# Optimization experiments

Hardware: AMD Instinct MI355X
Metric: run time of the kernel (lower is better)

## Reference

```python
import jax, jax.numpy as jnp
import numpy as np
import math

B, S, D = 2, 2048, 1024
N_HEAD = 16
EPS = 1e-6

def setup_inputs() -> dict:
    key = jax.random.key(0)
    ks = jax.random.split(key, 12)
    def lin(k):
        kw, kb = jax.random.split(k)
        scale = 1.0 / math.sqrt(D)
        W = jax.random.uniform(kw, (D, D), jnp.float32, -scale, scale)
        b = jax.random.uniform(kb, (D,), jnp.float32, -scale, scale)
        return W, b
    Wq, bq = lin(ks[0]); Wk, bk = lin(ks[1]); Wv, bv = lin(ks[2]); Wo, bo = lin(ks[3])
    return {
        'query': jax.random.normal(ks[4], (B, S, D), jnp.float32),
        'key':   jax.random.normal(ks[5], (B, S, D), jnp.float32),
        'value': jax.random.normal(ks[6], (B, S, D), jnp.float32),
        'mask':  jnp.ones((B, S, S), jnp.int32),
        'Wq': Wq, 'bq': bq, 'Wk': Wk, 'bk': bk, 'Wv': Wv, 'bv': bv,
        'Wo': Wo, 'bo': bo,
        'gamma': jnp.ones((D,), jnp.float32),
        'beta':  jnp.zeros((D,), jnp.float32),
    }

def reference(query, key, value, mask, Wq, bq, Wk, bk, Wv, bv, Wo, bo, gamma, beta):
    b, s, dm = query.shape
    h = N_HEAD
    d = dm // h
    residual = query
    # projections (torch Linear: x @ W.T + b) -> [b, h, s, d]
    def proj(x, W, bias):
        return (x @ W.T + bias).reshape(b, -1, h, d).transpose(0, 2, 1, 3)
    q = proj(query, Wq, bq)
    k = proj(key, Wk, bk)
    v = proj(value, Wv, bv)
    scores = jnp.einsum('bhqd,bhkd->bhqk', q, k) / jnp.sqrt(jnp.float32(d))
    scores = jnp.where(mask[:, None, :, :] == 0, jnp.float32(-1e9), scores)
    p_attn = jax.nn.softmax(scores, axis=-1)  # dropout is identity in eval/reference
    x = jnp.einsum('bhqk,bhkd->bhqd', p_attn, v)
    x = x.transpose(0, 2, 1, 3).reshape(b, -1, h * d)
    x = x @ Wo.T + bo
    x = x + residual
    # LayerNorm with unbiased std and (std + eps) denominator, as in source
    mean = jnp.mean(x, axis=-1, keepdims=True)
    std = jnp.std(x, axis=-1, keepdims=True, ddof=1)
    return gamma * (x - mean) / (std + EPS) + beta
```

## Files before the change

kernel.cpp:

```cpp
#include <hip/hip_runtime.h>
#include <hip/hip_bf16.h>
#include <math.h>
#include <stdint.h>

#define BATCH 2
#define SEQ   2048
#define DMODEL 1024
#define NHEAD 16
#define HDIM  64
#define NROWS (BATCH*SEQ)
#define EPS   1e-6f
#define QSCALE 0.1803368801111204f

typedef float f32x4 __attribute__((ext_vector_type(4)));
typedef short s16x8 __attribute__((ext_vector_type(8)));

#define OFF_XQ 0
#define OFF_XK 4194304
#define OFF_XV 8388608
#define OFF_WQ 12582912
#define OFF_WK 13631488
#define OFF_WV 14680064
#define OFF_WO 15728640
#define OFF_QB 16777216
#define OFF_KB 20971520
#define OFF_VT 25165824
#define OFF_CM 29360128
#define OFF_MS 29884416

__device__ __forceinline__ unsigned short f2bf(float x) {
    unsigned int u = __builtin_bit_cast(unsigned int, x);
    u += 0x7fff + ((u >> 16) & 1);
    return (unsigned short)(u >> 16);
}

__device__ __forceinline__ void gl_lds16(const void* g, void* l) {
    __builtin_amdgcn_global_load_lds(
        (const __attribute__((address_space(1))) unsigned int*)g,
        (__attribute__((address_space(3))) unsigned int*)(unsigned int)(unsigned long long)l,
        16, 0, 0);
}

__global__ __launch_bounds__(256) void conv_all_kernel(
    const float* __restrict__ q, const float* __restrict__ k, const float* __restrict__ v,
    const float* __restrict__ wq, const float* __restrict__ wk, const float* __restrict__ wv,
    const float* __restrict__ wo, unsigned short* __restrict__ ws)
{
    if (blockIdx.x == 0 && threadIdx.x < 32)
        ((unsigned int*)(ws + OFF_MS))[threadIdx.x] = 0;
    size_t t = ((size_t)blockIdx.x * 256 + threadIdx.x) * 4;
    const float* src; unsigned short* dst; size_t off;
    if (t < 4194304)       { src = q;  dst = ws + OFF_XQ; off = t; }
    else if (t < 8388608)  { src = k;  dst = ws + OFF_XK; off = t - 4194304; }
    else if (t < 12582912) { src = v;  dst = ws + OFF_XV; off = t - 8388608; }
    else if (t < 13631488) { src = wq; dst = ws + OFF_WQ; off = t - 12582912; }
    else if (t < 14680064) { src = wk; dst = ws + OFF_WK; off = t - 13631488; }
    else if (t < 15728640) { src = wv; dst = ws + OFF_WV; off = t - 14680064; }
    else                   { src = wo; dst = ws + OFF_WO; off = t - 15728640; }
    float4 x = *(const float4*)&src[off];
    ushort4 o;
    o.x = f2bf(x.x); o.y = f2bf(x.y); o.z = f2bf(x.z); o.w = f2bf(x.w);
    *(ushort4*)&dst[off] = o;
}

__global__ __launch_bounds__(256) void mask_compress_kernel(
    const int* __restrict__ mask, unsigned long long* __restrict__ cm,
    unsigned int* __restrict__ msum)
{
    int t = blockIdx.x * 256 + threadIdx.x;
    int s  = t & 2047;
    int kb = (t >> 11) & 31;
    int b  = t >> 16;
    const int* mp = mask + ((size_t)b * SEQ + s) * SEQ + kb * 64;
    unsigned long long bits = 0;
    #pragma unroll
    for (int i = 0; i < 16; i++) {
        int4 m4 = *(const int4*)&mp[i * 4];
        unsigned long long nib =
            (unsigned long long)((m4.x != 0) | ((m4.y != 0) << 1) |
                                 ((m4.z != 0) << 2) | ((m4.w != 0) << 3));
        bits |= nib << (i * 4);
    }
    cm[((size_t)b * 32 + kb) * SEQ + s] = bits;
    if (bits != ~0ull)
        atomicOr(&msum[(b << 4) | (s >> 7)], 1u << kb);
}

__device__ __forceinline__ void gemm_body(
    const unsigned short* A, const unsigned short* W, int r0, int c0,
    unsigned short* As, unsigned short* Bs, f32x4 acc[4][4])
{
    const int tid  = threadIdx.x;
    const int wave = tid >> 6, lane = tid & 63;
    const int quad = lane >> 4, l15 = lane & 15;
    const int wr = wave >> 1, wc = wave & 1;
    for (int k0 = 0; k0 < DMODEL; k0 += 64) {
        __syncthreads();
        #pragma unroll
        for (int r = 0; r < 4; r++) {
            int f = r * 4096 + tid * 16;
            int row = f >> 7, cb = f & 127;
            gl_lds16((const char*)A + (size_t)(r0 + row) * 2048 + k0 * 2 + cb,
                     (char*)As + r * 4096 + wave * 1024);
            gl_lds16((const char*)W + (size_t)(c0 + row) * 2048 + k0 * 2 + cb,
                     (char*)Bs + r * 4096 + wave * 1024);
        }
        __syncthreads();
        #pragma unroll
        for (int ks = 0; ks < 2; ks++) {
            s16x8 a[4], b[4];
            #pragma unroll
            for (int mt = 0; mt < 4; mt++)
                a[mt] = *(const s16x8*)((const char*)As + (wr*64 + mt*16 + l15) * 128 + ks*64 + quad*16);
            #pragma unroll
            for (int nt = 0; nt < 4; nt++)
                b[nt] = *(const s16x8*)((const char*)Bs + (wc*64 + nt*16 + l15) * 128 + ks*64 + quad*16);
            #pragma unroll
            for (int mt = 0; mt < 4; mt++)
                #pragma unroll
                for (int nt = 0; nt < 4; nt++)
                    acc[mt][nt] = __builtin_amdgcn_mfma_f32_16x16x32_bf16(a[mt], b[nt], acc[mt][nt], 0, 0, 0);
        }
    }
}

__global__ __launch_bounds__(256) void qkv_gemm_kernel(
    unsigned short* __restrict__ ws,
    const float* __restrict__ bq, const float* __restrict__ bk, const float* __restrict__ bv)
{
    __shared__ __align__(16) unsigned short As[8192];
    __shared__ __align__(16) unsigned short Bs[8192];
    const int z = blockIdx.z;
    const unsigned short *A, *W;
    int r0, c0;
    if (z != 2) {
        A = ws + (size_t)z * 4194304;
        W = ws + OFF_WQ + (size_t)z * 1048576;
        r0 = blockIdx.x * 128; c0 = blockIdx.y * 128;
    } else {
        A = ws + OFF_WV;
        W = ws + OFF_XV;
        r0 = blockIdx.y * 128; c0 = blockIdx.x * 128;
    }
    const float* bias = (z == 0) ? bq : (z == 1 ? bk : bv);
    unsigned short* outp = ws + OFF_QB + (size_t)z * 4194304;
    const float scale = (z == 0) ? QSCALE : 1.0f;

    f32x4 acc[4][4] = {};
    gemm_body(A, W, r0, c0, As, Bs, acc);

    const int lane = threadIdx.x & 63, wave = threadIdx.x >> 6;
    const int quad = lane >> 4, l15 = lane & 15;
    const int wr = wave >> 1, wc = wave & 1;
    if (z != 2) {
        float bias_v[4];
        #pragma unroll
        for (int nt = 0; nt < 4; nt++) bias_v[nt] = bias[c0 + wc*64 + nt*16 + l15];
        #pragma unroll
        for (int mt = 0; mt < 4; mt++) {
            #pragma unroll
            for (int nt = 0; nt < 4; nt++) {
                int c = c0 + wc*64 + nt*16 + l15;
                int hh = c >> 6, dd = c & 63;
                #pragma unroll
                for (int reg = 0; reg < 4; reg++) {
                    int r = r0 + wr*64 + mt*16 + quad*4 + reg;
                    int bb = r >> 11, ss = r & (SEQ - 1);
                    float val = (acc[mt][nt][reg] + bias_v[nt]) * scale;
                    outp[(((size_t)(bb*NHEAD + hh)) * SEQ + ss) * HDIM + dd] = f2bf(val);
                }
            }
        }
    } else {
        #pragma unroll
        for (int mt = 0; mt < 4; mt++) {
            #pragma unroll
            for (int reg = 0; reg < 4; reg++) {
                int f = r0 + wr*64 + mt*16 + quad*4 + reg;
                int hh = f >> 6, dd = f & 63;
                float bfv = bias[f];
                #pragma unroll
                for (int nt = 0; nt < 4; nt++) {
                    int r = c0 + wc*64 + nt*16 + l15;
                    int bb = r >> 11, ss = r & (SEQ - 1);
                    outp[(((size_t)(bb*NHEAD + hh)) * HDIM + dd) * SEQ + ss] =
                        f2bf(acc[mt][nt][reg] + bfv);
                }
            }
        }
    }
}

__global__ __launch_bounds__(256) void oproj_gemm_kernel(
    const unsigned short* __restrict__ ws, const float* __restrict__ bo,
    const float* __restrict__ resid, float* __restrict__ outf)
{
    __shared__ __align__(16) unsigned short As[8192];
    __shared__ __align__(16) unsigned short Bs[8192];
    const unsigned short* A = ws + OFF_XQ;
    const unsigned short* W = ws + OFF_WO;
    const int r0 = blockIdx.x * 128, c0 = blockIdx.y * 128;

    f32x4 acc[4][4] = {};
    gemm_body(A, W, r0, c0, (unsigned short*)As, (unsigned short*)Bs, acc);

    const int lane = threadIdx.x & 63, wave = threadIdx.x >> 6;
    const int quad = lane >> 4, l15 = lane & 15;
    const int wr = wave >> 1, wc = wave & 1;
    #pragma unroll
    for (int mt = 0; mt < 4; mt++) {
        #pragma unroll
        for (int nt = 0; nt < 4; nt++) {
            int c = c0 + wc*64 + nt*16 + l15;
            float bv = bo[c];
            #pragma unroll
            for (int reg = 0; reg < 4; reg++) {
                int r = r0 + wr*64 + mt*16 + quad*4 + reg;
                size_t idx = (size_t)r * DMODEL + c;
                outf[idx] = acc[mt][nt][reg] + bv + resid[idx];
            }
        }
    }
}

__global__ __launch_bounds__(512) void attn_mfma_kernel(
    const unsigned short* __restrict__ ws,
    const unsigned long long* __restrict__ cmask,
    const unsigned int* __restrict__ msum,
    unsigned short* __restrict__ ab)
{
    const int tid  = threadIdx.x;
    const int wave = tid >> 6, lane = tid & 63;
    const int quad = lane >> 4, l15 = lane & 15;
    const int h = blockIdx.y, b = blockIdx.z;
    const int qw = blockIdx.x * 128 + wave * 16;

    const char* qh = (const char*)(ws + OFF_QB + ((size_t)(b*NHEAD + h)) * SEQ * HDIM);
    const char* kh = (const char*)(ws + OFF_KB + ((size_t)(b*NHEAD + h)) * SEQ * HDIM);
    const char* vh = (const char*)(ws + OFF_VT + ((size_t)(b*NHEAD + h)) * SEQ * HDIM);

    __shared__ __align__(16) char Ks[2][8192];
    __shared__ __align__(16) char Vs[2][8192];
    __shared__ __align__(16) unsigned short Pl[8][16 * 72];
    unsigned short* Pw = Pl[wave];

    const unsigned int chunkflags = msum[(b << 4) | blockIdx.x];

    const int srow = tid >> 3;
    const int sgrp = ((tid & 7) - srow) & 7;

    #define STAGE(bf, k0)                                                       \
        do {                                                                    \
            gl_lds16(kh + (size_t)((k0) + srow) * 128 + sgrp * 16,              \
                     Ks[bf] + wave * 1024);                                     \
            gl_lds16(vh + (size_t)srow * 4096 + (size_t)(k0) * 2 + sgrp * 16,   \
                     Vs[bf] + wave * 1024);                                     \
        } while (0)

    s16x8 qa[2];
    #pragma unroll
    for (int ks = 0; ks < 2; ks++)
        qa[ks] = *(const s16x8*)(qh + (size_t)(qw + l15) * 128 + ks*64 + quad*16);

    s16x8 onesf;
    {
        short so = (short)0x3F80;
        if (l15 == 0) onesf = (s16x8){so, so, so, so, so, so, so, so};
        else          onesf = (s16x8){0, 0, 0, 0, 0, 0, 0, 0};
    }

    f32x4 o[4], lsum = {0.f, 0.f, 0.f, 0.f};
    #pragma unroll
    for (int nt = 0; nt < 4; nt++) o[nt] = (f32x4){0.f, 0.f, 0.f, 0.f};

    STAGE(0, 0);
    int bf = 0;
    for (int k0 = 0; k0 < SEQ; k0 += 64) {
        __syncthreads();
        if (k0 + 64 < SEQ) STAGE(bf ^ 1, k0 + 64);

        const char* Kb = Ks[bf];
        const char* Vb = Vs[bf];
        f32x4 s[4];
        #pragma unroll
        for (int nt = 0; nt < 4; nt++) {
            int key = nt*16 + l15;
            s16x8 kf0 = *(const s16x8*)(Kb + key*128 + ((quad     + key) & 7) * 16);
            s16x8 kf1 = *(const s16x8*)(Kb + key*128 + ((4 + quad + key) & 7) * 16);
            f32x4 z = {0.f, 0.f, 0.f, 0.f};
            s[nt] = __builtin_amdgcn_mfma_f32_16x16x32_bf16(qa[0], kf0, z, 0, 0, 0);
            s[nt] = __builtin_amdgcn_mfma_f32_16x16x32_bf16(qa[1], kf1, s[nt], 0, 0, 0);
        }
        if (chunkflags & (1u << (k0 >> 6))) {
            const unsigned long long* cmp =
                cmask + ((size_t)b*32 + (k0 >> 6)) * SEQ + qw + quad*4;
            #pragma unroll
            for (int reg = 0; reg < 4; reg++) {
                unsigned long long cm = cmp[reg];
                if (cm != ~0ull) {
                    #pragma unroll
                    for (int nt = 0; nt < 4; nt++) {
                        int n = nt*16 + l15;
                        if (!((cm >> n) & 1)) s[nt][reg] = -1e9f;
                    }
                }
            }
        }
        #pragma unroll
        for (int nt = 0; nt < 4; nt++)
            #pragma unroll
            for (int reg = 0; reg < 4; reg++) {
                float pv = exp2f(s[nt][reg]);
                Pw[(quad*4 + reg) * 72 + nt*16 + l15] =
                    (unsigned short)(__builtin_bit_cast(unsigned int, pv) >> 16);
            }
        #pragma unroll
        for (int ks = 0; ks < 2; ks++) {
            s16x8 pa = *(const s16x8*)((const char*)Pw + l15 * 144 + ks*64 + quad*16);
            lsum = __builtin_amdgcn_mfma_f32_16x16x32_bf16(pa, onesf, lsum, 0, 0, 0);
            #pragma unroll
            for (int nt = 0; nt < 4; nt++) {
                int d = nt*16 + l15;
                s16x8 vf = *(const s16x8*)(Vb + d*128 + ((ks*4 + quad + d) & 7) * 16);
                o[nt] = __builtin_amdgcn_mfma_f32_16x16x32_bf16(pa, vf, o[nt], 0, 0, 0);
            }
        }
        bf ^= 1;
    }
    #undef STAGE
    #pragma unroll
    for (int reg = 0; reg < 4; reg++) {
        float lv = __shfl(lsum[reg], lane & 48);
        float inv = 1.f / lv;
        int sg = qw + quad*4 + reg;
        #pragma unroll
        for (int nt = 0; nt < 4; nt++) {
            size_t idx = ((size_t)b * SEQ + sg) * DMODEL + h*HDIM + nt*16 + l15;
            ab[idx] = f2bf(o[nt][reg] * inv);
        }
    }
}

__global__ __launch_bounds__(256) void ln_kernel(
    float* __restrict__ x, const float* __restrict__ gamma,
    const float* __restrict__ beta)
{
    const int row = blockIdx.x;
    const int tid = threadIdx.x;
    float4 vals = *(const float4*)&x[(size_t)row * DMODEL + tid * 4];
    float s  = vals.x + vals.y + vals.z + vals.w;
    float ss = vals.x*vals.x + vals.y*vals.y + vals.z*vals.z + vals.w*vals.w;
    #pragma unroll
    for (int off = 32; off > 0; off >>= 1) {
        s  += __shfl_down(s, off);
        ss += __shfl_down(ss, off);
    }
    __shared__ float sbuf[4], ssbuf[4];
    __shared__ float mean_s, inv_s;
    if ((tid & 63) == 0) { sbuf[tid >> 6] = s; ssbuf[tid >> 6] = ss; }
    __syncthreads();
    if (tid == 0) {
        float S1 = 0.f, S2 = 0.f;
        #pragma unroll
        for (int i = 0; i < 4; i++) { S1 += sbuf[i]; S2 += ssbuf[i]; }
        float mean = S1 * (1.0f / DMODEL);
        float var  = (S2 - (float)DMODEL * mean * mean) * (1.0f / (DMODEL - 1));
        float sd   = sqrtf(fmaxf(var, 0.f));
        mean_s = mean;
        inv_s  = 1.f / (sd + EPS);
    }
    __syncthreads();
    float4 g  = *(const float4*)&gamma[tid * 4];
    float4 bt = *(const float4*)&beta[tid * 4];
    float4 o;
    o.x = g.x * (vals.x - mean_s) * inv_s + bt.x;
    o.y = g.y * (vals.y - mean_s) * inv_s + bt.y;
    o.z = g.z * (vals.z - mean_s) * inv_s + bt.z;
    o.w = g.w * (vals.w - mean_s) * inv_s + bt.w;
    *(float4*)&x[(size_t)row * DMODEL + tid * 4] = o;
}

extern "C" void kernel_launch(void* const* d_in, const int* in_sizes, int n_in,
                              void* d_out, int out_size, void* d_ws, size_t ws_size,
                              hipStream_t stream) {
    const float* query = (const float*)d_in[0];
    const float* key   = (const float*)d_in[1];
    const float* value = (const float*)d_in[2];
    const int*   mask  = (const int*)d_in[3];
    const float* Wq = (const float*)d_in[4];  const float* bq = (const float*)d_in[5];
    const float* Wk = (const float*)d_in[6];  const float* bk = (const float*)d_in[7];
    const float* Wv = (const float*)d_in[8];  const float* bv = (const float*)d_in[9];
    const float* Wo = (const float*)d_in[10]; const float* bo = (const float*)d_in[11];
    const float* gamma = (const float*)d_in[12];
    const float* beta  = (const float*)d_in[13];
    float* out = (float*)d_out;

    unsigned short* ws = (unsigned short*)d_ws;
    unsigned long long* cmask = (unsigned long long*)(ws + OFF_CM);
    unsigned int* msum = (unsigned int*)(ws + OFF_MS);

    conv_all_kernel<<<16384, 256, 0, stream>>>(query, key, value, Wq, Wk, Wv, Wo, ws);
    mask_compress_kernel<<<512, 256, 0, stream>>>(mask, cmask, msum);
    qkv_gemm_kernel<<<dim3(32, 8, 3), 256, 0, stream>>>(ws, bq, bk, bv);
    attn_mfma_kernel<<<dim3(SEQ/128, NHEAD, BATCH), 512, 0, stream>>>(ws, cmask, msum, ws + OFF_XQ);
    oproj_gemm_kernel<<<dim3(32, 8), 256, 0, stream>>>(ws, bo, query, out);
    ln_kernel<<<NROWS, 256, 0, stream>>>(out, gamma, beta);
}
```

Baseline: 289.4 us.

## Fuse mask compression into conversion, split-K out-proj, widen attention wave tiles

Result: slower. 314.0 us (+8.5%).

```diff
diff --git a/kernel.cpp b/kernel.cpp
--- a/kernel.cpp
+++ b/kernel.cpp
@@ -44,10 +44,30 @@
 __global__ __launch_bounds__(256) void conv_all_kernel(
     const float* __restrict__ q, const float* __restrict__ k, const float* __restrict__ v,
     const float* __restrict__ wq, const float* __restrict__ wk, const float* __restrict__ wv,
-    const float* __restrict__ wo, unsigned short* __restrict__ ws)
-{
-    if (blockIdx.x == 0 && threadIdx.x < 32)
-        ((unsigned int*)(ws + OFF_MS))[threadIdx.x] = 0;
+    const float* __restrict__ wo, unsigned short* __restrict__ ws,
+    const int* __restrict__ mask, unsigned long long* __restrict__ cm,
+    unsigned int* __restrict__ msum)
+{
+    if (blockIdx.x >= 16384) {
+        int t = (blockIdx.x - 16384) * 256 + threadIdx.x;
+        int s  = t & 2047;
+        int kb = (t >> 11) & 31;
+        int b  = t >> 16;
+        const int* mp = mask + ((size_t)b * SEQ + s) * SEQ + kb * 64;
+        unsigned long long bits = 0;
+        #pragma unroll
+        for (int i = 0; i < 16; i++) {
+            int4 m4 = *(const int4*)&mp[i * 4];
+            unsigned long long nib =
+                (unsigned long long)((m4.x != 0) | ((m4.y != 0) << 1) |
+                                     ((m4.z != 0) << 2) | ((m4.w != 0) << 3));
+            bits |= nib << (i * 4);
+        }
+        cm[((size_t)b * 32 + kb) * SEQ + s] = bits;
+        if (bits != ~0ull)
+            atomicOr(&msum[(b << 4) | (s >> 7)], 1u << kb);
+        return;
+    }
     size_t t = ((size_t)blockIdx.x * 256 + threadIdx.x) * 4;
     const float* src; unsigned short* dst; size_t off;
     if (t < 4194304)       { src = q;  dst = ws + OFF_XQ; off = t; }
@@ -63,38 +83,15 @@
     *(ushort4*)&dst[off] = o;
 }
 
-__global__ __launch_bounds__(256) void mask_compress_kernel(
-    const int* __restrict__ mask, unsigned long long* __restrict__ cm,
-    unsigned int* __restrict__ msum)
-{
-    int t = blockIdx.x * 256 + threadIdx.x;
-    int s  = t & 2047;
-    int kb = (t >> 11) & 31;
-    int b  = t >> 16;
-    const int* mp = mask + ((size_t)b * SEQ + s) * SEQ + kb * 64;
-    unsigned long long bits = 0;
-    #pragma unroll
-    for (int i = 0; i < 16; i++) {
-        int4 m4 = *(const int4*)&mp[i * 4];
-        unsigned long long nib =
-            (unsigned long long)((m4.x != 0) | ((m4.y != 0) << 1) |
-                                 ((m4.z != 0) << 2) | ((m4.w != 0) << 3));
-        bits |= nib << (i * 4);
-    }
-    cm[((size_t)b * 32 + kb) * SEQ + s] = bits;
-    if (bits != ~0ull)
-        atomicOr(&msum[(b << 4) | (s >> 7)], 1u << kb);
-}
-
 __device__ __forceinline__ void gemm_body(
     const unsigned short* A, const unsigned short* W, int r0, int c0,
-    unsigned short* As, unsigned short* Bs, f32x4 acc[4][4])
+    int kbeg, int kend, unsigned short* As, unsigned short* Bs, f32x4 acc[4][4])
 {
     const int tid  = threadIdx.x;
     const int wave = tid >> 6, lane = tid & 63;
     const int quad = lane >> 4, l15 = lane & 15;
     const int wr = wave >> 1, wc = wave & 1;
-    for (int k0 = 0; k0 < DMODEL; k0 += 64) {
+    for (int k0 = kbeg; k0 < kend; k0 += 64) {
         __syncthreads();
         #pragma unroll
         for (int r = 0; r < 4; r++) {
@@ -147,7 +144,7 @@
     const float scale = (z == 0) ? QSCALE : 1.0f;
 
     f32x4 acc[4][4] = {};
-    gemm_body(A, W, r0, c0, As, Bs, acc);
+    gemm_body(A, W, r0, c0, 0, DMODEL, As, Bs, acc);
 
     const int lane = threadIdx.x & 63, wave = threadIdx.x >> 6;
     const int quad = lane >> 4, l15 = lane & 15;
@@ -192,18 +189,20 @@
 }
 
 __global__ __launch_bounds__(256) void oproj_gemm_kernel(
-    const unsigned short* __restrict__ ws, const float* __restrict__ bo,
-    const float* __restrict__ resid, float* __restrict__ outf)
+    const unsigned short* __restrict__ ws,
+    float* __restrict__ p0, float* __restrict__ p1)
 {
     __shared__ __align__(16) unsigned short As[8192];
     __shared__ __align__(16) unsigned short Bs[8192];
     const unsigned short* A = ws + OFF_XQ;
     const unsigned short* W = ws + OFF_WO;
     const int r0 = blockIdx.x * 128, c0 = blockIdx.y * 128;
+    const int z = blockIdx.z;
 
     f32x4 acc[4][4] = {};
-    gemm_body(A, W, r0, c0, (unsigned short*)As, (unsigned short*)Bs, acc);
-
+    gemm_body(A, W, r0, c0, z * 512, z * 512 + 512, As, Bs, acc);
+
+    float* outp = z ? p1 : p0;
     const int lane = threadIdx.x & 63, wave = threadIdx.x >> 6;
     const int quad = lane >> 4, l15 = lane & 15;
     const int wr = wave >> 1, wc = wave & 1;
@@ -212,18 +211,16 @@
         #pragma unroll
         for (int nt = 0; nt < 4; nt++) {
             int c = c0 + wc*64 + nt*16 + l15;
-            float bv = bo[c];
             #pragma unroll
             for (int reg = 0; reg < 4; reg++) {
                 int r = r0 + wr*64 + mt*16 + quad*4 + reg;
-                size_t idx = (size_t)r * DMODEL + c;
-                outf[idx] = acc[mt][nt][reg] + bv + resid[idx];
-            }
-        }
-    }
-}
-
-__global__ __launch_bounds__(512) void attn_mfma_kernel(
+                outp[(size_t)r * DMODEL + c] = acc[mt][nt][reg];
+            }
+        }
+    }
+}
+
+__global__ __launch_bounds__(256) void attn_mfma_kernel(
     const unsigned short* __restrict__ ws,
     const unsigned long long* __restrict__ cmask,
     const unsigned int* __restrict__ msum,
@@ -233,7 +230,7 @@
     const int wave = tid >> 6, lane = tid & 63;
     const int quad = lane >> 4, l15 = lane & 15;
     const int h = blockIdx.y, b = blockIdx.z;
-    const int qw = blockIdx.x * 128 + wave * 16;
+    const int qw = blockIdx.x * 128 + wave * 32;
 
     const char* qh = (const char*)(ws + OFF_QB + ((size_t)(b*NHEAD + h)) * SEQ * HDIM);
     const char* kh = (const char*)(ws + OFF_KB + ((size_t)(b*NHEAD + h)) * SEQ * HDIM);
@@ -241,26 +238,32 @@
 
     __shared__ __align__(16) char Ks[2][8192];
     __shared__ __align__(16) char Vs[2][8192];
-    __shared__ __align__(16) unsigned short Pl[8][16 * 72];
+    __shared__ __align__(16) unsigned short Pl[4][32 * 72];
     unsigned short* Pw = Pl[wave];
 
     const unsigned int chunkflags = msum[(b << 4) | blockIdx.x];
 
     const int srow = tid >> 3;
-    const int sgrp = ((tid & 7) - srow) & 7;
-
-    #define STAGE(bf, k0)                                                       \
-        do {                                                                    \
-            gl_lds16(kh + (size_t)((k0) + srow) * 128 + sgrp * 16,              \
-                     Ks[bf] + wave * 1024);                                     \
-            gl_lds16(vh + (size_t)srow * 4096 + (size_t)(k0) * 2 + sgrp * 16,   \
-                     Vs[bf] + wave * 1024);                                     \
+    const int g0   = ((tid & 7) - srow) & 7;
+
+    #define STAGE(bf, k0)                                                          \
+        do {                                                                       \
+            gl_lds16(kh + (size_t)((k0) + srow) * 128 + g0 * 16,                   \
+                     Ks[bf] + wave * 1024);                                        \
+            gl_lds16(kh + (size_t)((k0) + srow + 32) * 128 + g0 * 16,              \
+                     Ks[bf] + 4096 + wave * 1024);                                 \
+            gl_lds16(vh + (size_t)srow * 4096 + (size_t)(k0) * 2 + g0 * 16,        \
+                     Vs[bf] + wave * 1024);                                        \
+            gl_lds16(vh + (size_t)(srow + 32) * 4096 + (size_t)(k0) * 2 + g0 * 16, \
+                     Vs[bf] + 4096 + wave * 1024);                                 \
         } while (0)
 
-    s16x8 qa[2];
+    s16x8 qa[2][2];
     #pragma unroll
-    for (int ks = 0; ks < 2; ks++)
-        qa[ks] = *(const s16x8*)(qh + (size_t)(qw + l15) * 128 + ks*64 + quad*16);
+    for (int mt = 0; mt < 2; mt++)
+        #pragma unroll
+        for (int ks = 0; ks < 2; ks++)
+            qa[mt][ks] = *(const s16x8*)(qh + (size_t)(qw + mt*16 + l15) * 128 + ks*64 + quad*16);
 
     s16x8 onesf;
     {
@@ -269,9 +272,13 @@
         else          onesf = (s16x8){0, 0, 0, 0, 0, 0, 0, 0};
     }
 
-    f32x4 o[4], lsum = {0.f, 0.f, 0.f, 0.f};
+    f32x4 o[2][4], lsum[2];
     #pragma unroll
-    for (int nt = 0; nt < 4; nt++) o[nt] = (f32x4){0.f, 0.f, 0.f, 0.f};
+    for (int mt = 0; mt < 2; mt++) {
+        lsum[mt] = (f32x4){0.f, 0.f, 0.f, 0.f};
+        #pragma unroll
+        for (int nt = 0; nt < 4; nt++) o[mt][nt] = (f32x4){0.f, 0.f, 0.f, 0.f};
+    }
 
     STAGE(0, 0);
     int bf = 0;
@@ -281,73 +288,99 @@
 
         const char* Kb = Ks[bf];
         const char* Vb = Vs[bf];
-        f32x4 s[4];
+        f32x4 s[2][4];
         #pragma unroll
         for (int nt = 0; nt < 4; nt++) {
             int key = nt*16 + l15;
             s16x8 kf0 = *(const s16x8*)(Kb + key*128 + ((quad     + key) & 7) * 16);
             s16x8 kf1 = *(const s16x8*)(Kb + key*128 + ((4 + quad + key) & 7) * 16);
-            f32x4 z = {0.f, 0.f, 0.f, 0.f};
-            s[nt] = __builtin_amdgcn_mfma_f32_16x16x32_bf16(qa[0], kf0, z, 0, 0, 0);
-            s[nt] = __builtin_amdgcn_mfma_f32_16x16x32_bf16(qa[1], kf1, s[nt], 0, 0, 0);
+            #pragma unroll
+            for (int mt = 0; mt < 2; mt++) {
+                f32x4 z = {0.f, 0.f, 0.f, 0.f};
+                s[mt][nt] = __builtin_amdgcn_mfma_f32_16x16x32_bf16(qa[mt][0], kf0, z, 0, 0, 0);
+                s[mt][nt] = __builtin_amdgcn_mfma_f32_16x16x32_bf16(qa[mt][1], kf1, s[mt][nt], 0, 0, 0);
+            }
         }
         if (chunkflags & (1u << (k0 >> 6))) {
             const unsigned long long* cmp =
                 cmask + ((size_t)b*32 + (k0 >> 6)) * SEQ + qw + quad*4;
             #pragma unroll
-            for (int reg = 0; reg < 4; reg++) {
-                unsigned long long cm = cmp[reg];
-                if (cm != ~0ull) {
-                    #pragma unroll
-                    for (int nt = 0; nt < 4; nt++) {
-                        int n = nt*16 + l15;
-                        if (!((cm >> n) & 1)) s[nt][reg] = -1e9f;
+            for (int mt = 0; mt < 2; mt++)
+                #pragma unroll
+                for (int reg = 0; reg < 4; reg++) {
+                    unsigned long long cm = cmp[mt*16 + reg];
+                    if (cm != ~0ull) {
+                        #pragma unroll
+                        for (int nt = 0; nt < 4; nt++) {
+                            int n = nt*16 + l15;
+                            if (!((cm >> n) & 1)) s[mt][nt][reg] = -1e9f;
+                        }
                     }
                 }
-            }
-        }
-        #pragma unroll
-        for (int nt = 0; nt < 4; nt++)
-            #pragma unroll
-            for (int reg = 0; reg < 4; reg++) {
-                float pv = exp2f(s[nt][reg]);
-                Pw[(quad*4 + reg) * 72 + nt*16 + l15] =
-                    (unsigned short)(__builtin_bit_cast(unsigned int, pv) >> 16);
-            }
+        }
+        #pragma unroll
+        for (int mt = 0; mt < 2; mt++)
+            #pragma unroll
+            for (int nt = 0; nt < 4; nt++)
+                #pragma unroll
+                for (int reg = 0; reg < 4; reg++) {
+                    float pv = exp2f(s[mt][nt][reg]);
+                    Pw[(mt*16 + quad*4 + reg) * 72 + nt*16 + l15] =
+                        (unsigned short)(__builtin_bit_cast(unsigned int, pv) >> 16);
+                }
         #pragma unroll
         for (int ks = 0; ks < 2; ks++) {
-            s16x8 pa = *(const s16x8*)((const char*)Pw + l15 * 144 + ks*64 + quad*16);
-            lsum = __builtin_amdgcn_mfma_f32_16x16x32_bf16(pa, onesf, lsum, 0, 0, 0);
+            s16x8 pa[2];
+            #pragma unroll
+            for (int mt = 0; mt < 2; mt++) {
+                pa[mt] = *(const s16x8*)((const char*)Pw + (mt*16 + l15) * 144 + ks*64 + quad*16);
+                lsum[mt] = __builtin_amdgcn_mfma_f32_16x16x32_bf16(pa[mt], onesf, lsum[mt], 0, 0, 0);
+            }
             #pragma unroll
             for (int nt = 0; nt < 4; nt++) {
                 int d = nt*16 + l15;
                 s16x8 vf = *(const s16x8*)(Vb + d*128 + ((ks*4 + quad + d) & 7) * 16);
-                o[nt] = __builtin_amdgcn_mfma_f32_16x16x32_bf16(pa, vf, o[nt], 0, 0, 0);
+                #pragma unroll
+                for (int mt = 0; mt < 2; mt++)
+                    o[mt][nt] = __builtin_amdgcn_mfma_f32_16x16x32_bf16(pa[mt], vf, o[mt][nt], 0, 0, 0);
             }
         }
         bf ^= 1;
     }
     #undef STAGE
     #pragma unroll
-    for (int reg = 0; reg < 4; reg++) {
-        float lv = __shfl(lsum[reg], lane & 48);
-        float inv = 1.f / lv;
-        int sg = qw + quad*4 + reg;
-        #pragma unroll
-        for (int nt = 0; nt < 4; nt++) {
-            size_t idx = ((size_t)b * SEQ + sg) * DMODEL + h*HDIM + nt*16 + l15;
-            ab[idx] = f2bf(o[nt][reg] * inv);
-        }
-    }
+    for (int mt = 0; mt < 2; mt++)
+        #pragma unroll
+        for (int reg = 0; reg < 4; reg++) {
+            float lv = __shfl(lsum[mt][reg], lane & 48);
+            float inv = 1.f / lv;
+            int sg = qw + mt*16 + quad*4 + reg;
+            #pragma unroll
+            for (int nt = 0; nt < 4; nt++) {
+                size_t idx = ((size_t)b * SEQ + sg) * DMODEL + h*HDIM + nt*16 + l15;
+                ab[idx] = f2bf(o[mt][nt][reg] * inv);
+            }
+        }
 }
 
 __global__ __launch_bounds__(256) void ln_kernel(
-    float* __restrict__ x, const float* __restrict__ gamma,
-    const float* __restrict__ beta)
+    const float* __restrict__ p0, const float* __restrict__ p1,
+    const float* __restrict__ resid, const float* __restrict__ bo,
+    const float* __restrict__ gamma, const float* __restrict__ beta,
+    float* __restrict__ out)
 {
     const int row = blockIdx.x;
     const int tid = threadIdx.x;
-    float4 vals = *(const float4*)&x[(size_t)row * DMODEL + tid * 4];
+    const size_t i = (size_t)row * DMODEL + tid * 4;
+    float4 a  = *(const float4*)&p0[i];
+    float4 b2 = *(const float4*)&p1[i];
+    float4 r  = *(const float4*)&resid[i];
+    float4 bb = *(const float4*)&bo[tid * 4];
+    float4 vals;
+    vals.x = a.x + b2.x + r.x + bb.x;
+    vals.y = a.y + b2.y + r.y + bb.y;
+    vals.z = a.z + b2.z + r.z + bb.z;
+    vals.w = a.w + b2.w + r.w + bb.w;
     float s  = vals.x + vals.y + vals.z + vals.w;
     float ss = vals.x*vals.x + vals.y*vals.y + vals.z*vals.z + vals.w*vals.w;
     #pragma unroll
@@ -362,7 +395,7 @@
     if (tid == 0) {
         float S1 = 0.f, S2 = 0.f;
         #pragma unroll
-        for (int i = 0; i < 4; i++) { S1 += sbuf[i]; S2 += ssbuf[i]; }
+        for (int i2 = 0; i2 < 4; i2++) { S1 += sbuf[i2]; S2 += ssbuf[i2]; }
         float mean = S1 * (1.0f / DMODEL);
         float var  = (S2 - (float)DMODEL * mean * mean) * (1.0f / (DMODEL - 1));
         float sd   = sqrtf(fmaxf(var, 0.f));
@@ -377,7 +410,7 @@
     o.y = g.y * (vals.y - mean_s) * inv_s + bt.y;
     o.z = g.z * (vals.z - mean_s) * inv_s + bt.z;
     o.w = g.w * (vals.w - mean_s) * inv_s + bt.w;
-    *(float4*)&x[(size_t)row * DMODEL + tid * 4] = o;
+    *(float4*)&out[i] = o;
 }
 
 extern "C" void kernel_launch(void* const* d_in, const int* in_sizes, int n_in,
@@ -398,11 +431,14 @@
     unsigned short* ws = (unsigned short*)d_ws;
     unsigned long long* cmask = (unsigned long long*)(ws + OFF_CM);
     unsigned int* msum = (unsigned int*)(ws + OFF_MS);
-
-    conv_all_kernel<<<16384, 256, 0, stream>>>(query, key, value, Wq, Wk, Wv, Wo, ws);
-    mask_compress_kernel<<<512, 256, 0, stream>>>(mask, cmask, msum);
+    float* p0 = (float*)(ws + OFF_XK);
+    float* p1 = (float*)(ws + OFF_QB);
+
+    hipMemsetAsync(msum, 0, 128, stream);
+    conv_all_kernel<<<16896, 256, 0, stream>>>(query, key, value, Wq, Wk, Wv, Wo,
+                                               ws, mask, cmask, msum);
     qkv_gemm_kernel<<<dim3(32, 8, 3), 256, 0, stream>>>(ws, bq, bk, bv);
-    attn_mfma_kernel<<<dim3(SEQ/128, NHEAD, BATCH), 512, 0, stream>>>(ws, cmask, msum, ws + OFF_XQ);
-    oproj_gemm_kernel<<<dim3(32, 8), 256, 0, stream>>>(ws, bo, query, out);
-    ln_kernel<<<NROWS, 256, 0, stream>>>(out, gamma, beta);
-}
+    attn_mfma_kernel<<<dim3(SEQ/128, NHEAD, BATCH), 256, 0, stream>>>(ws, cmask, msum, ws + OFF_XQ);
+    oproj_gemm_kernel<<<dim3(32, 8, 2), 256, 0, stream>>>(ws, p0, p1);
+    ln_kernel<<<NROWS, 256, 0, stream>>>(p0, p1, query, bo, gamma, beta, out);
+}
```
